# Kernel optimization log

Measured on AMD Instinct MI355X. Metric: run time of the kernel, lower is better.

Reference implementation:

```python
import jax, jax.numpy as jnp
import numpy as np

B, S, T = 4, 1024, 1024
CTX, QIN, C, H = 1024, 1024, 1024, 16
HD = C // H  # per-head channels


def setup_inputs() -> dict:
    key = jax.random.key(0)
    ks = jax.random.split(key, 12)
    s = 0.02
    return {
        "query": jax.random.normal(ks[0], (B, S, QIN), jnp.float32),
        "key": jax.random.normal(ks[1], (B, T, CTX), jnp.float32),
        "value": jax.random.normal(ks[2], (B, T, CTX), jnp.float32),
        "mask": jax.random.randint(ks[3], (B, S, T), 0, 2).astype(bool),
        "Wq": jax.random.normal(ks[4], (C, QIN), jnp.float32) * s,
        "bq": jax.random.normal(ks[5], (C,), jnp.float32) * s,
        "Wk": jax.random.normal(ks[6], (C, CTX), jnp.float32) * s,
        "bk": jax.random.normal(ks[7], (C,), jnp.float32) * s,
        "Wv": jax.random.normal(ks[8], (C, CTX), jnp.float32) * s,
        "bv": jax.random.normal(ks[9], (C,), jnp.float32) * s,
        "Wo": jax.random.normal(ks[10], (C, C), jnp.float32) * s,
        "bo": jax.random.normal(ks[11], (C,), jnp.float32) * s,
    }


def reference(query, key, value, mask, Wq, bq, Wk, bk, Wv, bv, Wo, bo):
    b, s, _ = query.shape
    t = key.shape[1]
    c = Wq.shape[0]
    h, hd = H, c // H
    q = (query @ Wq.T + bq).reshape(b, s, h, hd)
    k = (key @ Wk.T + bk).reshape(b, t, h, hd)
    v = (value @ Wv.T + bv).reshape(b, t, h, hd)
    # [B,H,S,T] scores, scaled by 1/sqrt(head_dim)
    score = jnp.einsum('bshd,bthd->bhst', q, k) * (hd ** -0.5)
    # masked_fill_(~mask[:, None, 0:1], -inf): mask key positions via row 0
    score = jnp.where(mask[:, None, 0:1], score, -jnp.inf)
    weights = jax.nn.softmax(score, axis=-1)
    out = jnp.einsum('bhst,bthd->bshd', weights, v).reshape(b, s, c)
    out = out @ Wo.T + bo
    out = out * mask[..., 0:1].astype(out.dtype)
    return out
```

## Files before the change

### kernel.cpp

```cpp
#include <hip/hip_runtime.h>
#include <stdint.h>

#define Bb  4
#define Ss  1024
#define Tt  1024
#define Cc  1024
#define Hh  16
#define HDd 64
#define Kk  1024

typedef __bf16 bf16;
typedef __bf16 bf16x8 __attribute__((ext_vector_type(8)));
typedef float  f32x4  __attribute__((ext_vector_type(4)));
typedef __attribute__((address_space(1))) uint32_t gu32;
typedef __attribute__((address_space(3))) uint32_t lu32;

__device__ __forceinline__ void load_lds16(const bf16* g, bf16* l) {
    __builtin_amdgcn_global_load_lds((gu32*)g, (lu32*)l, 16, 0, 0);
}

#define BARRIER_LDS() do {                                    \
    asm volatile("s_waitcnt lgkmcnt(0)" ::: "memory");        \
    __builtin_amdgcn_s_barrier();                             \
} while (0)

#define BARRIER_VM() do {                                     \
    asm volatile("s_waitcnt vmcnt(0)" ::: "memory");          \
    __builtin_amdgcn_s_barrier();                             \
} while (0)

__global__ void cvt8(const float* __restrict__ s0, const float* __restrict__ s1,
                     const float* __restrict__ s2, const float* __restrict__ s3,
                     const float* __restrict__ s4, const float* __restrict__ s5,
                     const float* __restrict__ s6,
                     bf16* __restrict__ d0, bf16* __restrict__ d1,
                     bf16* __restrict__ d2, bf16* __restrict__ d3,
                     bf16* __restrict__ d4, bf16* __restrict__ d5,
                     bf16* __restrict__ d6)
{
    const float* s; bf16* d; int n;
    switch (blockIdx.y) {
        case 0: s = s0; d = d0; n = Bb * Ss * Kk; break;
        case 1: s = s1; d = d1; n = Bb * Ss * Kk; break;
        case 2: s = s2; d = d2; n = Bb * Ss * Kk; break;
        case 3: s = s3; d = d3; n = Cc * Kk; break;
        case 4: s = s4; d = d4; n = Cc * Kk; break;
        case 5: s = s5; d = d5; n = Cc * Kk; break;
        default: s = s6; d = d6; n = Cc * Kk; break;
    }
    const int i = (blockIdx.x * blockDim.x + threadIdx.x) * 8;
    if (i >= n) return;
    const float4 a = *(const float4*)(s + i);
    const float4 c = *(const float4*)(s + i + 4);
    bf16x8 o;
    o[0] = (bf16)a.x; o[1] = (bf16)a.y; o[2] = (bf16)a.z; o[3] = (bf16)a.w;
    o[4] = (bf16)c.x; o[5] = (bf16)c.y; o[6] = (bf16)c.z; o[7] = (bf16)c.w;
    *(bf16x8*)(d + i) = o;
}

__device__ __forceinline__ void mainloop_128x64_2ph(
    const bf16* __restrict__ Ab, const bf16* __restrict__ Wb,
    bf16* As, bf16* Bs, f32x4 acc[4][2])
{
    const int tid  = threadIdx.x;
    const int wid  = tid >> 6;
    const int lane = tid & 63;
    const int l16  = lane & 15;
    const int quad = lane >> 4;
    const int wm   = wid >> 1;
    const int wn   = wid & 1;
    const int r8   = lane >> 3;
    const int ssw  = ((lane & 7) ^ r8) * 8;

    auto stage = [&](int buf, int k0) {
        bf16* Asb = As + buf * (128 * 64);
        bf16* Bsb = Bs + buf * (64 * 64);
#pragma unroll
        for (int p = 0; p < 4; p++) {
            const int rb = wid * 32 + p * 8;
            load_lds16(Ab + (size_t)(rb + r8) * Kk + k0 + ssw, Asb + rb * 64);
        }
#pragma unroll
        for (int p = 0; p < 2; p++) {
            const int rb = wid * 16 + p * 8;
            load_lds16(Wb + (size_t)(rb + r8) * Kk + k0 + ssw, Bsb + rb * 64);
        }
    };

    auto compute = [&](const bf16* Asb, const bf16* Bsb) {
#pragma unroll
        for (int kh = 0; kh < 2; kh++) {
            bf16x8 af[4], bw[2];
#pragma unroll
            for (int i = 0; i < 4; i++)
                af[i] = *(const bf16x8*)(Asb + (wm * 64 + i * 16 + l16) * 64 +
                                         (((kh * 4 + quad) ^ (l16 & 7)) * 8));
#pragma unroll
            for (int j = 0; j < 2; j++)
                bw[j] = *(const bf16x8*)(Bsb + (wn * 32 + j * 16 + l16) * 64 +
                                         (((kh * 4 + quad) ^ (l16 & 7)) * 8));
#pragma unroll
            for (int i = 0; i < 4; i++)
#pragma unroll
                for (int j = 0; j < 2; j++)
                    acc[i][j] = __builtin_amdgcn_mfma_f32_16x16x32_bf16(af[i], bw[j], acc[i][j], 0, 0, 0);
        }
    };

    stage(0, 0);
    BARRIER_VM();

    for (int k0 = 0; k0 < Kk; k0 += 128) {
        stage(1, k0 + 64);
        compute(As, Bs);
        BARRIER_VM();
        if (k0 + 128 < Kk) stage(0, k0 + 128);
        compute(As + 128 * 64, Bs + 64 * 64);
        BARRIER_VM();
    }
}

__global__ __launch_bounds__(256)
void gemm_qkv(const bf16* __restrict__ Aq, const bf16* __restrict__ Ak, const bf16* __restrict__ Av,
              const bf16* __restrict__ Wq, const bf16* __restrict__ Wk, const bf16* __restrict__ Wv,
              const float* __restrict__ bq, const float* __restrict__ bk, const float* __restrict__ bv,
              bf16* __restrict__ Oq, bf16* __restrict__ Ok, bf16* __restrict__ Ov)
{
    __shared__ __align__(16) bf16 As[2 * 128 * 64];
    __shared__ __align__(16) bf16 Bs[2 * 64 * 64];
    const int z = blockIdx.z;
    const bf16*  A    = (z == 0) ? Aq : (z == 1) ? Ak : Av;
    const bf16*  W    = (z == 0) ? Wq : (z == 1) ? Wk : Wv;
    const float* bias = (z == 0) ? bq : (z == 1) ? bk : bv;
    bf16*        O    = (z == 0) ? Oq : (z == 1) ? Ok : Ov;

    f32x4 acc[4][2];
    const f32x4 z4 = {0.f, 0.f, 0.f, 0.f};
#pragma unroll
    for (int i = 0; i < 4; i++)
#pragma unroll
        for (int j = 0; j < 2; j++) acc[i][j] = z4;

    mainloop_128x64_2ph(A + (size_t)blockIdx.x * 128 * Kk,
                        W + (size_t)blockIdx.y * 64 * Kk, As, Bs, acc);

    const int tid = threadIdx.x;
    const int wid = tid >> 6, lane = tid & 63;
    const int l16 = lane & 15, quad = lane >> 4;
    const int wm = wid >> 1, wn = wid & 1;
    const int row0 = blockIdx.x * 128 + wm * 64;
    const int col0 = blockIdx.y * 64 + wn * 32;
#pragma unroll
    for (int j = 0; j < 2; j++) {
        const int col = col0 + j * 16 + l16;
        const float bj = bias[col];
        const int h = col >> 6, d = col & 63;
#pragma unroll
        for (int i = 0; i < 4; i++) {
#pragma unroll
            for (int r = 0; r < 4; r++) {
                const int row = row0 + i * 16 + quad * 4 + r;
                const int b = row >> 10, s = row & 1023;
                const bf16 val = (bf16)(acc[i][j][r] + bj);
                if (z == 2) {
                    Ov[((size_t)((b * Hh + h) * HDd + d)) * Tt + s] = val;
                } else {
                    O[((size_t)(b * Hh + h) * Ss + s) * HDd + d] = val;
                }
            }
        }
    }
}

__global__ __launch_bounds__(256)
void gemm_out(const bf16* __restrict__ A, const bf16* __restrict__ W,
              const float* __restrict__ bias, const int* __restrict__ mask,
              float* __restrict__ out)
{
    __shared__ __align__(16) bf16 As[2 * 128 * 64];
    __shared__ __align__(16) bf16 Bs[2 * 64 * 64];
    f32x4 acc[4][2];
    const f32x4 z4 = {0.f, 0.f, 0.f, 0.f};
#pragma unroll
    for (int i = 0; i < 4; i++)
#pragma unroll
        for (int j = 0; j < 2; j++) acc[i][j] = z4;

    mainloop_128x64_2ph(A + (size_t)blockIdx.x * 128 * Kk,
                        W + (size_t)blockIdx.y * 64 * Kk, As, Bs, acc);

    const int tid = threadIdx.x;
    const int wid = tid >> 6, lane = tid & 63;
    const int l16 = lane & 15, quad = lane >> 4;
    const int wm = wid >> 1, wn = wid & 1;
    const int row0 = blockIdx.x * 128 + wm * 64;
    const int col0 = blockIdx.y * 64 + wn * 32;
#pragma unroll
    for (int j = 0; j < 2; j++) {
        const int col = col0 + j * 16 + l16;
        const float bj = bias[col];
#pragma unroll
        for (int i = 0; i < 4; i++) {
#pragma unroll
            for (int r = 0; r < 4; r++) {
                const int row = row0 + i * 16 + quad * 4 + r;
                const float mval = (mask[(size_t)row * Tt] != 0) ? 1.f : 0.f;
                out[(size_t)row * Cc + col] = (acc[i][j][r] + bj) * mval;
            }
        }
    }
}

__global__ __launch_bounds__(256, 4)
void attn(const bf16* __restrict__ Q, const bf16* __restrict__ Kp, const bf16* __restrict__ Vt,
          const int* __restrict__ mask, bf16* __restrict__ X)
{
    __shared__ __align__(16) bf16 Ks[64 * 64];
    __shared__ __align__(16) bf16 Vs[64 * 64];
    __shared__ __align__(16) bf16 Ps[4][16 * 72];
    const int g   = blockIdx.x;
    const int xcd = g & 7, idx = g >> 3;
    const int bh  = xcd * 8 + (idx >> 4);
    const int qblk = idx & 15;
    const int b = bh >> 4, h = bh & 15;
    const int tid = threadIdx.x, wid = tid >> 6, lane = tid & 63;
    const int l16 = lane & 15, quad = lane >> 4;
    const bf16* Qbh = Q  + (size_t)bh * Ss * HDd;
    const bf16* Kbh = Kp + (size_t)bh * Tt * HDd;
    const bf16* Vbh = Vt + (size_t)bh * HDd * Tt;
    const int*  mb  = mask + (size_t)b * Ss * Tt;
    const int q0 = qblk * 64 + wid * 16;
    bf16* Psw = &Ps[wid][0];

    const bf16x8 qf0 = *(const bf16x8*)(Qbh + (size_t)(q0 + l16) * HDd + quad * 8);
    const bf16x8 qf1 = *(const bf16x8*)(Qbh + (size_t)(q0 + l16) * HDd + 32 + quad * 8);

    float ls[4];
    f32x4 o[4];
    const f32x4 z4 = {0.f, 0.f, 0.f, 0.f};
#pragma unroll
    for (int r = 0; r < 4; r++) ls[r] = 0.f;
#pragma unroll
    for (int dblk = 0; dblk < 4; dblk++) o[dblk] = z4;

    const int srow = lane >> 3;
    const int schk = lane & 7;
    const int sswz = (schk ^ srow) * 8;
    const int c80 = wid * 2, c81 = wid * 2 + 1;

    const bf16* kg0 = Kbh + (size_t)(c80 * 8 + srow) * HDd + sswz;
    const bf16* kg1 = Kbh + (size_t)(c81 * 8 + srow) * HDd + sswz;
    const bf16* vg0 = Vbh + (size_t)(c80 * 8 + srow) * Tt + sswz;
    const bf16* vg1 = Vbh + (size_t)(c81 * 8 + srow) * Tt + sswz;
    bf16* kd0 = Ks + c80 * 512 + lane * 8;
    bf16* kd1 = Ks + c81 * 512 + lane * 8;
    bf16* vd0 = Vs + c80 * 512 + lane * 8;
    bf16* vd1 = Vs + c81 * 512 + lane * 8;

    bf16x8 ka0, ka1, va0, va1;
    bf16x8 kb0, kb1, vb0, vb1;
    int mA0, mA1, mA2, mA3, mB0, mB1, mB2, mB3;

#define LOADA(KT) do { const int _kt = (KT);                          \
    ka0 = *(const bf16x8*)(kg0 + (size_t)_kt * HDd);                  \
    ka1 = *(const bf16x8*)(kg1 + (size_t)_kt * HDd);                  \
    va0 = *(const bf16x8*)(vg0 + _kt);                                \
    va1 = *(const bf16x8*)(vg1 + _kt);                                \
    mA0 = mb[_kt + l16];      mA1 = mb[_kt + 16 + l16];               \
    mA2 = mb[_kt + 32 + l16]; mA3 = mb[_kt + 48 + l16]; } while (0)
#define LOADB(KT) do { const int _kt = (KT);                          \
    kb0 = *(const bf16x8*)(kg0 + (size_t)_kt * HDd);                  \
    kb1 = *(const bf16x8*)(kg1 + (size_t)_kt * HDd);                  \
    vb0 = *(const bf16x8*)(vg0 + _kt);                                \
    vb1 = *(const bf16x8*)(vg1 + _kt);                                \
    mB0 = mb[_kt + l16];      mB1 = mb[_kt + 16 + l16];               \
    mB2 = mb[_kt + 32 + l16]; mB3 = mb[_kt + 48 + l16]; } while (0)
#define STOREA() do {                                                 \
    *(bf16x8*)kd0 = ka0; *(bf16x8*)kd1 = ka1;                         \
    *(bf16x8*)vd0 = va0; *(bf16x8*)vd1 = va1; } while (0)
#define STOREB() do {                                                 \
    *(bf16x8*)kd0 = kb0; *(bf16x8*)kd1 = kb1;                         \
    *(bf16x8*)vd0 = vb0; *(bf16x8*)vd1 = vb1; } while (0)

    auto compute = [&](int m0, int m1, int m2, int m3) {
        f32x4 sc[4];
#pragma unroll
        for (int nb = 0; nb < 4; nb++) sc[nb] = z4;
#pragma unroll
        for (int nb = 0; nb < 4; nb++) {
            const bf16* krow = Ks + (nb * 16 + l16) * 64;
            const bf16x8 kf0 = *(const bf16x8*)(krow + ((quad       ^ (l16 & 7)) * 8));
            const bf16x8 kf1 = *(const bf16x8*)(krow + (((4 + quad) ^ (l16 & 7)) * 8));
            sc[nb] = __builtin_amdgcn_mfma_f32_16x16x32_bf16(qf0, kf0, sc[nb], 0, 0, 0);
            sc[nb] = __builtin_amdgcn_mfma_f32_16x16x32_bf16(qf1, kf1, sc[nb], 0, 0, 0);
        }

        const int mm[4] = {m0, m1, m2, m3};
#pragma unroll
        for (int nb = 0; nb < 4; nb++) {
            const float madd = mm[nb] ? 0.f : -1e30f;
#pragma unroll
            for (int r = 0; r < 4; r++) {
                const float p = __expf(sc[nb][r] * 0.125f + madd);
                ls[r] += p;
                Psw[(quad * 4 + r) * 72 + nb * 16 + l16] = (bf16)p;
            }
        }

#pragma unroll
        for (int kh = 0; kh < 2; kh++) {
            const bf16x8 pf = *(const bf16x8*)(Psw + l16 * 72 + kh * 32 + quad * 8);
#pragma unroll
            for (int dblk = 0; dblk < 4; dblk++) {
                const bf16x8 vf = *(const bf16x8*)(Vs + (dblk * 16 + l16) * 64 +
                                                   (((kh * 4 + quad) ^ (l16 & 7)) * 8));
                o[dblk] = __builtin_amdgcn_mfma_f32_16x16x32_bf16(pf, vf, o[dblk], 0, 0, 0);
            }
        }
    };

    LOADA(0);

    for (int kt = 0; kt < Tt; kt += 128) {
        BARRIER_LDS();
        LOADB(kt + 64);
        STOREA();
        BARRIER_LDS();
        compute(mA0, mA1, mA2, mA3);

        BARRIER_LDS();
        LOADA((kt + 128 < Tt) ? (kt + 128) : (Tt - 64));
        STOREB();
        BARRIER_LDS();
        compute(mB0, mB1, mB2, mB3);
    }
#undef LOADA
#undef LOADB
#undef STOREA
#undef STOREB

#pragma unroll
    for (int off = 1; off <= 8; off <<= 1)
#pragma unroll
        for (int r = 0; r < 4; r++)
            ls[r] += __shfl_xor(ls[r], off, 64);
    float inv[4];
#pragma unroll
    for (int r = 0; r < 4; r++) inv[r] = 1.f / ls[r];

#pragma unroll
    for (int dblk = 0; dblk < 4; dblk++) {
#pragma unroll
        for (int r = 0; r < 4; r++) {
            const int srow_q = q0 + quad * 4 + r;
            const int d = dblk * 16 + l16;
            X[(size_t)(b * Ss + srow_q) * Cc + h * HDd + d] = (bf16)(o[dblk][r] * inv[r]);
        }
    }
}

extern "C" void kernel_launch(void* const* d_in, const int* in_sizes, int n_in,
                              void* d_out, int out_size, void* d_ws, size_t ws_size,
                              hipStream_t stream)
{
    const float* query = (const float*)d_in[0];
    const float* key   = (const float*)d_in[1];
    const float* value = (const float*)d_in[2];
    const int*   mask  = (const int*)d_in[3];
    const float* Wq = (const float*)d_in[4];
    const float* bq = (const float*)d_in[5];
    const float* Wk = (const float*)d_in[6];
    const float* bk = (const float*)d_in[7];
    const float* Wv = (const float*)d_in[8];
    const float* bv = (const float*)d_in[9];
    const float* Wo = (const float*)d_in[10];
    const float* bo = (const float*)d_in[11];
    float* out = (float*)d_out;

    char* ws = (char*)d_ws;
    const size_t MB = 1024 * 1024;
    bf16* qb  = (bf16*)(ws + 0 * MB);
    bf16* kb  = (bf16*)(ws + 8 * MB);
    bf16* vb  = (bf16*)(ws + 16 * MB);
    bf16* wqb = (bf16*)(ws + 24 * MB);
    bf16* wkb = (bf16*)(ws + 26 * MB);
    bf16* wvb = (bf16*)(ws + 28 * MB);
    bf16* wob = (bf16*)(ws + 30 * MB);
    bf16* Qp  = (bf16*)(ws + 32 * MB);
    bf16* Kpp = (bf16*)(ws + 40 * MB);
    bf16* Vtp = (bf16*)(ws + 48 * MB);
    bf16* Xb  = (bf16*)(ws + 56 * MB);

    cvt8<<<dim3(2048, 7), 256, 0, stream>>>(query, key, value, Wq, Wk, Wv, Wo,
                                            qb, kb, vb, wqb, wkb, wvb, wob);
    gemm_qkv<<<dim3(32, 16, 3), 256, 0, stream>>>(qb, kb, vb, wqb, wkb, wvb,
                                                  bq, bk, bv, Qp, Kpp, Vtp);
    attn<<<dim3(1024), 256, 0, stream>>>(Qp, Kpp, Vtp, mask, Xb);
    gemm_out<<<dim3(32, 16), 256, 0, stream>>>(Xb, wob, bo, mask, out);
}
```

Measured before the change: 232.6 us.

## Replace double-buffered GEMM mainloop with single-buffer register-prefetch pipeline

The GEMM mainloop for the QKV and output projections moves from two LDS buffers to one. Each iteration reads the whole 64-wide K tile into registers, waits at a barrier, starts the global-to-LDS load for the next tile, and then runs the MFMAs from registers. This halves LDS use per block, which may let more blocks fit on a CU, and lets the next load overlap the MFMAs. The cost is more registers for the fragments and an extra barrier per K step.

Result: faster. 223.1 us (-4.1%).

```diff
diff --git a/kernel.cpp b/kernel.cpp
--- a/kernel.cpp
+++ b/kernel.cpp
@@ -58,7 +58,7 @@
     *(bf16x8*)(d + i) = o;
 }
 
-__device__ __forceinline__ void mainloop_128x64_2ph(
+__device__ __forceinline__ void mainloop_128x64_pf(
     const bf16* __restrict__ Ab, const bf16* __restrict__ Wb,
     bf16* As, bf16* Bs, f32x4 acc[4][2])
 {
@@ -72,50 +72,44 @@
     const int r8   = lane >> 3;
     const int ssw  = ((lane & 7) ^ r8) * 8;
 
-    auto stage = [&](int buf, int k0) {
-        bf16* Asb = As + buf * (128 * 64);
-        bf16* Bsb = Bs + buf * (64 * 64);
+    auto stage = [&](int k0) {
 #pragma unroll
         for (int p = 0; p < 4; p++) {
             const int rb = wid * 32 + p * 8;
-            load_lds16(Ab + (size_t)(rb + r8) * Kk + k0 + ssw, Asb + rb * 64);
+            load_lds16(Ab + (size_t)(rb + r8) * Kk + k0 + ssw, As + rb * 64);
         }
 #pragma unroll
         for (int p = 0; p < 2; p++) {
             const int rb = wid * 16 + p * 8;
-            load_lds16(Wb + (size_t)(rb + r8) * Kk + k0 + ssw, Bsb + rb * 64);
+            load_lds16(Wb + (size_t)(rb + r8) * Kk + k0 + ssw, Bs + rb * 64);
         }
     };
 
-    auto compute = [&](const bf16* Asb, const bf16* Bsb) {
+    stage(0);
+    BARRIER_VM();
+
+    for (int k0 = 0; k0 < Kk; k0 += 64) {
+        bf16x8 af[2][4], bw[2][2];
 #pragma unroll
         for (int kh = 0; kh < 2; kh++) {
-            bf16x8 af[4], bw[2];
 #pragma unroll
             for (int i = 0; i < 4; i++)
-                af[i] = *(const bf16x8*)(Asb + (wm * 64 + i * 16 + l16) * 64 +
-                                         (((kh * 4 + quad) ^ (l16 & 7)) * 8));
+                af[kh][i] = *(const bf16x8*)(As + (wm * 64 + i * 16 + l16) * 64 +
+                                             (((kh * 4 + quad) ^ (l16 & 7)) * 8));
 #pragma unroll
             for (int j = 0; j < 2; j++)
-                bw[j] = *(const bf16x8*)(Bsb + (wn * 32 + j * 16 + l16) * 64 +
-                                         (((kh * 4 + quad) ^ (l16 & 7)) * 8));
+                bw[kh][j] = *(const bf16x8*)(Bs + (wn * 32 + j * 16 + l16) * 64 +
+                                             (((kh * 4 + quad) ^ (l16 & 7)) * 8));
+        }
+        BARRIER_LDS();
+        if (k0 + 64 < Kk) stage(k0 + 64);
+#pragma unroll
+        for (int kh = 0; kh < 2; kh++)
 #pragma unroll
             for (int i = 0; i < 4; i++)
 #pragma unroll
                 for (int j = 0; j < 2; j++)
-                    acc[i][j] = __builtin_amdgcn_mfma_f32_16x16x32_bf16(af[i], bw[j], acc[i][j], 0, 0, 0);
-        }
-    };
-
-    stage(0, 0);
-    BARRIER_VM();
-
-    for (int k0 = 0; k0 < Kk; k0 += 128) {
-        stage(1, k0 + 64);
-        compute(As, Bs);
-        BARRIER_VM();
-        if (k0 + 128 < Kk) stage(0, k0 + 128);
-        compute(As + 128 * 64, Bs + 64 * 64);
+                    acc[i][j] = __builtin_amdgcn_mfma_f32_16x16x32_bf16(af[kh][i], bw[kh][j], acc[i][j], 0, 0, 0);
         BARRIER_VM();
     }
 }
@@ -126,8 +120,8 @@
               const float* __restrict__ bq, const float* __restrict__ bk, const float* __restrict__ bv,
               bf16* __restrict__ Oq, bf16* __restrict__ Ok, bf16* __restrict__ Ov)
 {
-    __shared__ __align__(16) bf16 As[2 * 128 * 64];
-    __shared__ __align__(16) bf16 Bs[2 * 64 * 64];
+    __shared__ __align__(16) bf16 As[128 * 64];
+    __shared__ __align__(16) bf16 Bs[64 * 64];
     const int z = blockIdx.z;
     const bf16*  A    = (z == 0) ? Aq : (z == 1) ? Ak : Av;
     const bf16*  W    = (z == 0) ? Wq : (z == 1) ? Wk : Wv;
@@ -141,8 +135,8 @@
 #pragma unroll
         for (int j = 0; j < 2; j++) acc[i][j] = z4;
 
-    mainloop_128x64_2ph(A + (size_t)blockIdx.x * 128 * Kk,
-                        W + (size_t)blockIdx.y * 64 * Kk, As, Bs, acc);
+    mainloop_128x64_pf(A + (size_t)blockIdx.x * 128 * Kk,
+                       W + (size_t)blockIdx.y * 64 * Kk, As, Bs, acc);
 
     const int tid = threadIdx.x;
     const int wid = tid >> 6, lane = tid & 63;
@@ -177,8 +171,8 @@
               const float* __restrict__ bias, const int* __restrict__ mask,
               float* __restrict__ out)
 {
-    __shared__ __align__(16) bf16 As[2 * 128 * 64];
-    __shared__ __align__(16) bf16 Bs[2 * 64 * 64];
+    __shared__ __align__(16) bf16 As[128 * 64];
+    __shared__ __align__(16) bf16 Bs[64 * 64];
     f32x4 acc[4][2];
     const f32x4 z4 = {0.f, 0.f, 0.f, 0.f};
 #pragma unroll
@@ -186,8 +180,8 @@
 #pragma unroll
         for (int j = 0; j < 2; j++) acc[i][j] = z4;
 
-    mainloop_128x64_2ph(A + (size_t)blockIdx.x * 128 * Kk,
-                        W + (size_t)blockIdx.y * 64 * Kk, As, Bs, acc);
+    mainloop_128x64_pf(A + (size_t)blockIdx.x * 128 * Kk,
+                       W + (size_t)blockIdx.y * 64 * Kk, As, Bs, acc);
 
     const int tid = threadIdx.x;
     const int wid = tid >> 6, lane = tid & 63;
```
